# Kernel optimization log

Measured on AMD Instinct MI355X. Metric: run time of the kernel, lower is better.

## Reference

```python
import jax, jax.numpy as jnp
import numpy as np

B, S, V, D, H, T = 16, 256, 32000, 512, 512, 50


def setup_inputs() -> dict:
    key = jax.random.key(0)
    ks = jax.random.split(key, 6)
    tokens = jax.random.randint(ks[0], (B, S), 0, V, dtype=jnp.int64)
    topic_probs = jax.random.uniform(ks[1], (B, S, T), dtype=jnp.float32)
    topic_probs = topic_probs / jnp.linalg.norm(topic_probs, axis=-1, keepdims=True)
    embed_table = jax.random.normal(ks[2], (V, D), dtype=jnp.float32) * 0.02
    lstm_kernel = jax.random.normal(ks[3], (T + D + H, 4 * H), dtype=jnp.float32) * 0.02
    lstm_bias = jnp.zeros((4 * H,), dtype=jnp.float32)
    dense_w = jax.random.normal(ks[4], (H, V), dtype=jnp.float32) * 0.02
    dense_b = jnp.zeros((V,), dtype=jnp.float32)
    return {"tokens": tokens, "topic_probs": topic_probs, "embed_table": embed_table,
            "lstm_kernel": lstm_kernel, "lstm_bias": lstm_bias,
            "dense_w": dense_w, "dense_b": dense_b}


def _lstm(xs, kernel, bias):
    # xs: [B, S, T+D]; TF LSTMCell gate order: i, j(cell cand), f, o; forget_bias=0.0
    h_dim = bias.shape[0] // 4
    b = xs.shape[0]

    def step(carry, xt):
        c, h = carry
        z = jnp.concatenate([xt, h], axis=-1) @ kernel + bias  # [B, 4H]
        i, j, f, o = jnp.split(z, 4, axis=-1)
        c = jax.nn.sigmoid(f) * c + jax.nn.sigmoid(i) * jnp.tanh(j)
        h = jax.nn.sigmoid(o) * jnp.tanh(c)
        return (c, h), h

    init = (jnp.zeros((b, h_dim), xs.dtype), jnp.zeros((b, h_dim), xs.dtype))
    _, hs = jax.lax.scan(step, init, jnp.swapaxes(xs, 0, 1))  # [S, B, H]
    return jnp.swapaxes(hs, 0, 1)


def reference(tokens, topic_probs, embed_table, lstm_kernel, lstm_bias, dense_w, dense_b):
    word_emb = embed_table[tokens]                         # [B, S, D]
    xs = jnp.concatenate([topic_probs, word_emb], axis=-1)  # [B, S, T+D]
    hs = _lstm(xs, lstm_kernel, lstm_bias)                 # [B, S, H]
    logits = hs @ dense_w + dense_b                        # [B, S, V]
    return logits
```

## Files before the change

### kernel.cpp

```cpp
#include <hip/hip_runtime.h>
#include <cstdint>
#include <cstddef>

#define B_ 16
#define S_ 256
#define V_ 32000
#define D_ 512
#define H_ 512
#define T_ 50
#define KX (T_ + D_)
#define G4 (4 * H_)
#define M_ (B_ * S_)

#define GBLK 64
#define NWRK 192
#define UPB 8
#define WST 512
#define NJT 32
#define NNT 250

typedef unsigned short u16;
typedef unsigned int u32;
typedef __attribute__((ext_vector_type(8))) short bf16x8;
typedef __attribute__((ext_vector_type(4))) float f32x4;
typedef __attribute__((ext_vector_type(4))) u16 u16x4;
typedef __attribute__((ext_vector_type(8))) u16 u16x8;
typedef __attribute__((ext_vector_type(4))) u32 u32x4;

__device__ __forceinline__ float sigmoidf_(float x) { return 1.f / (1.f + expf(-x)); }

__device__ __forceinline__ u16 f2bf_rne(float x) {
  u32 u = __float_as_uint(x);
  u32 r = (u + 0x7fffu + ((u >> 16) & 1u)) >> 16;
  return (u16)r;
}
__device__ __forceinline__ float bf2f(u16 h) { return __uint_as_float(((u32)h) << 16); }

__device__ __forceinline__ int swz(int row, int k) {
  return row * WST + (k ^ ((row & 7) << 3));
}

#define GLD_LDS16(g, l) __builtin_amdgcn_global_load_lds( \
    (const __attribute__((address_space(1))) void*)(g), \
    (__attribute__((address_space(3))) void*)(l), 16, 0, 0)

#define BM 128
#define BN 128
#define BK 16

__global__ __launch_bounds__(256) void proj_gemm(
    const int* __restrict__ tokens, const float* __restrict__ topic,
    const float* __restrict__ embed, const float* __restrict__ Wx,
    const float* __restrict__ bias, float* __restrict__ out) {
  __shared__ float As[BK][BM];
  __shared__ float Bs[BK][BN];
  const int tid = threadIdx.x;
  const int bm = blockIdx.y * BM;
  const int bn = blockIdx.x * BN;
  const int tx = tid & 15;
  const int ty = tid >> 4;
  float acc[8][8] = {};

  for (int k0 = 0; k0 < KX; k0 += BK) {
    {
      int r = tid >> 1;
      int kk = (tid & 1) * 8;
      int m = bm + r;
      int tok = tokens[m];
      #pragma unroll
      for (int i = 0; i < 8; ++i) {
        int kg = k0 + kk + i;
        float v = 0.f;
        if (kg < T_)       v = topic[(size_t)m * T_ + kg];
        else if (kg < KX)  v = embed[(size_t)tok * D_ + (kg - T_)];
        As[kk + i][r] = v;
      }
    }
    {
      int kk = tid >> 4;
      int nn = (tid & 15) * 8;
      int kg = k0 + kk;
      const float* Bp = Wx + (size_t)kg * G4 + bn + nn;
      #pragma unroll
      for (int i = 0; i < 8; ++i)
        Bs[kk][nn + i] = (kg < KX) ? Bp[i] : 0.f;
    }
    __syncthreads();
    #pragma unroll
    for (int k = 0; k < BK; ++k) {
      float a[8], bv[8];
      #pragma unroll
      for (int i = 0; i < 8; ++i) a[i] = As[k][ty * 8 + i];
      #pragma unroll
      for (int i = 0; i < 8; ++i) bv[i] = Bs[k][tx * 8 + i];
      #pragma unroll
      for (int i = 0; i < 8; ++i)
        #pragma unroll
        for (int j = 0; j < 8; ++j)
          acc[i][j] += a[i] * bv[j];
    }
    __syncthreads();
  }

  #pragma unroll
  for (int i = 0; i < 8; ++i) {
    int m = bm + ty * 8 + i;
    float* Cp = out + (size_t)m * G4 + bn + tx * 8;
    #pragma unroll
    for (int j = 0; j < 8; ++j)
      Cp[j] = acc[i][j] + bias[bn + tx * 8 + j];
  }
}

__global__ __launch_bounds__(256) void split_w_t(
    const float* __restrict__ W, u16* __restrict__ Whi, u16* __restrict__ Wlo) {
  __shared__ float tile[32][33];
  const int n0 = blockIdx.x * 32, k0 = blockIdx.y * 32;
  const int r = threadIdx.x >> 3;
  const int c4 = (threadIdx.x & 7) * 4;
  const float* src = W + (size_t)(k0 + r) * V_ + n0 + c4;
  #pragma unroll
  for (int i = 0; i < 4; ++i) tile[r][c4 + i] = src[i];
  __syncthreads();
  u16x4 hv, lv;
  #pragma unroll
  for (int i = 0; i < 4; ++i) {
    float x = tile[c4 + i][r];
    u16 h = f2bf_rne(x);
    hv[i] = h;
    lv[i] = f2bf_rne(x - bf2f(h));
  }
  size_t o = (size_t)(n0 + r) * 512 + k0 + c4;
  *(u16x4*)(Whi + o) = hv;
  *(u16x4*)(Wlo + o) = lv;
}

__global__ __launch_bounds__(256, 1) void fused_lstm_dense(
    const float* __restrict__ xs_proj, const float* __restrict__ Wh,
    u32* __restrict__ hpk,
    u32* __restrict__ Apk,
    u32* __restrict__ ctr,
    const u16* __restrict__ Bhi, const u16* __restrict__ Blo,
    const float* __restrict__ bias, float* __restrict__ out) {
  __shared__ u16 whi_l[32 * WST];
  __shared__ u16 wlo_l[32 * WST];
  __shared__ u16 hhi_l[16 * WST];
  __shared__ u16 hlo_l[16 * WST];
  __shared__ float zpart[4][16][34];
  __shared__ u16 Ah_l[128 * 32];
  __shared__ u16 Al_l[128 * 32];
  __shared__ u16 Bh_l[128 * 32];
  __shared__ u16 Bl_l[128 * 32];

  const int bid = blockIdx.x;
  const int tid = threadIdx.x;
  const int w = tid >> 6;
  const int lane = tid & 63;

  if (bid < GBLK) {
    const int u0 = bid * UPB;

    for (int idx = tid; idx < 32 * 512; idx += 256) {
      int c = idx & 31, k = idx >> 5;
      int gc = (c >> 3) * 512 + u0 + (c & 7);
      float v = Wh[(size_t)k * G4 + gc];
      u16 hi = f2bf_rne(v);
      int si = swz(c, k);
      whi_l[si] = hi;
      wlo_l[si] = f2bf_rne(v - bf2f(hi));
    }

    float c_reg = 0.f;
    const int rb = tid >> 3;
    const int rj = tid & 7;
    const int kb = (lane >> 4) * 8;
    const int l15 = lane & 15;

    for (int s = 0; s < S_; ++s) {
      float zi = 0.f, zj2 = 0.f, zf = 0.f, zo = 0.f;
      if (tid < 128) {
        const float* zp = xs_proj + ((size_t)rb * S_ + s) * G4 + u0 + rj;
        zi = zp[0]; zj2 = zp[512]; zf = zp[1024]; zo = zp[1536];
      }

      if (s > 0) {
        if (tid == 0) {
          const u32 tgt = 64u * (u32)s;
          while (__hip_atomic_load(ctr, __ATOMIC_RELAXED,
                                   __HIP_MEMORY_SCOPE_AGENT) < tgt)
            __builtin_amdgcn_s_sleep(1);
        }
        __syncthreads();
        asm volatile("" ::: "memory");
      }

      {
        const u32* src = hpk + (size_t)(s & 1) * 8192;
        u32 v[32];
        #pragma unroll
        for (int j = 0; j < 32; ++j)
          v[j] = __hip_atomic_load(src + tid + j * 256, __ATOMIC_RELAXED,
                                   __HIP_MEMORY_SCOPE_AGENT);
        #pragma unroll
        for (int j = 0; j < 32; ++j) {
          int idx = tid + j * 256;
          int b = idx >> 9, u = idx & 511;
          int si = swz(b, u);
          hhi_l[si] = (u16)(v[j] & 0xffffu);
          hlo_l[si] = (u16)(v[j] >> 16);
        }
      }
      __syncthreads();

      {
        f32x4 acc0 = {0.f, 0.f, 0.f, 0.f};
        f32x4 acc1 = {0.f, 0.f, 0.f, 0.f};
        #pragma unroll
        for (int ks = 0; ks < 4; ++ks) {
          const int k = w * 128 + ks * 32 + kb;
          const int ia = swz(l15, k);
          const int ib = swz(16 + l15, k);
          bf16x8 ah  = *(const bf16x8*)&hhi_l[ia];
          bf16x8 al  = *(const bf16x8*)&hlo_l[ia];
          bf16x8 b0h = *(const bf16x8*)&whi_l[ia];
          bf16x8 b0l = *(const bf16x8*)&wlo_l[ia];
          bf16x8 b1h = *(const bf16x8*)&whi_l[ib];
          bf16x8 b1l = *(const bf16x8*)&wlo_l[ib];
          acc0 = __builtin_amdgcn_mfma_f32_16x16x32_bf16(al, b0h, acc0, 0, 0, 0);
          acc0 = __builtin_amdgcn_mfma_f32_16x16x32_bf16(ah, b0l, acc0, 0, 0, 0);
          acc0 = __builtin_amdgcn_mfma_f32_16x16x32_bf16(ah, b0h, acc0, 0, 0, 0);
          acc1 = __builtin_amdgcn_mfma_f32_16x16x32_bf16(al, b1h, acc1, 0, 0, 0);
          acc1 = __builtin_amdgcn_mfma_f32_16x16x32_bf16(ah, b1l, acc1, 0, 0, 0);
          acc1 = __builtin_amdgcn_mfma_f32_16x16x32_bf16(ah, b1h, acc1, 0, 0, 0);
        }
        #pragma unroll
        for (int jj = 0; jj < 4; ++jj) {
          int r = (lane >> 4) * 4 + jj;
          zpart[w][r][l15] = acc0[jj];
          zpart[w][r][16 + l15] = acc1[jj];
        }
      }
      __syncthreads();

      if (tid < 128) {
        #pragma unroll
        for (int ww = 0; ww < 4; ++ww) {
          zi  += zpart[ww][rb][rj];
          zj2 += zpart[ww][rb][8 + rj];
          zf  += zpart[ww][rb][16 + rj];
          zo  += zpart[ww][rb][24 + rj];
        }
        float cc = sigmoidf_(zf) * c_reg + sigmoidf_(zi) * tanhf(zj2);
        c_reg = cc;
        float h = sigmoidf_(zo) * tanhf(cc);
        u16 hh = f2bf_rne(h);
        u16 hl = f2bf_rne(h - bf2f(hh));
        u32 pack = (u32)hh | ((u32)hl << 16);
        const int hoff = rb * 512 + u0 + rj;
        __hip_atomic_store(hpk + (size_t)((s + 1) & 1) * 8192 + hoff, pack,
                           __ATOMIC_RELAXED, __HIP_MEMORY_SCOPE_AGENT);
        const size_t ar = ((size_t)s * 16 + rb) * 512 + u0 + rj;
        __hip_atomic_store(Apk + ar, pack,
                           __ATOMIC_RELAXED, __HIP_MEMORY_SCOPE_AGENT);
      }
      asm volatile("s_waitcnt vmcnt(0)" ::: "memory");
      __syncthreads();

      if (tid == 0)
        __hip_atomic_fetch_add(ctr, 1u, __ATOMIC_RELAXED,
                               __HIP_MEMORY_SCOPE_AGENT);
    }
  } else {
    const int wid = bid - GBLK;
    const int wm = (w >> 1) * 64, wn = (w & 1) * 64;
    const int l15 = lane & 15;
    const int kb = (lane >> 4) * 8;
    const int lrow = lane >> 2;
    const int lkb = (lane & 3) * 8;
    const int r_ = tid >> 1;
    const int kh = (tid & 1) * 16;

    int lastj = -1;
    for (int t = wid; t < NJT * NNT; t += NWRK) {
      const int jt = t / NNT;
      const int n  = t - jt * NNT;
      if (jt != lastj) {
        if (tid == 0) {
          const u32 tgt = 512u * (u32)(jt + 1);
          while (__hip_atomic_load(ctr, __ATOMIC_RELAXED,
                                   __HIP_MEMORY_SCOPE_AGENT) < tgt)
            __builtin_amdgcn_s_sleep(32);
        }
        __syncthreads();
        asm volatile("" ::: "memory");
        lastj = jt;
      }

      const int bmA = jt * 128;
      const int bn = n * 128;
      f32x4 acc[4][4];
      #pragma unroll
      for (int m = 0; m < 4; ++m)
        #pragma unroll
        for (int q = 0; q < 4; ++q) acc[m][q] = (f32x4){0.f, 0.f, 0.f, 0.f};

      const u16* srcBh = Bhi + (size_t)bn * 512;
      const u16* srcBl = Blo + (size_t)bn * 512;

      for (int k0 = 0; k0 < 512; k0 += 32) {
        {
          const u32* ap = Apk + (size_t)(bmA + r_) * 512 + k0 + kh;
          u32x4 a0 = *(const u32x4*)(ap);
          u32x4 a1 = *(const u32x4*)(ap + 4);
          u32x4 a2 = *(const u32x4*)(ap + 8);
          u32x4 a3 = *(const u32x4*)(ap + 12);
          u16x8 h0, h1, l0, l1;
          #pragma unroll
          for (int i = 0; i < 4; ++i) {
            h0[i]   = (u16)(a0[i] & 0xffffu); l0[i]   = (u16)(a0[i] >> 16);
            h0[4+i] = (u16)(a1[i] & 0xffffu); l0[4+i] = (u16)(a1[i] >> 16);
            h1[i]   = (u16)(a2[i] & 0xffffu); l1[i]   = (u16)(a2[i] >> 16);
            h1[4+i] = (u16)(a3[i] & 0xffffu); l1[4+i] = (u16)(a3[i] >> 16);
          }
          *(u16x8*)&Ah_l[r_ * 32 + kh]     = h0;
          *(u16x8*)&Ah_l[r_ * 32 + kh + 8] = h1;
          *(u16x8*)&Al_l[r_ * 32 + kh]     = l0;
          *(u16x8*)&Al_l[r_ * 32 + kh + 8] = l1;
        }
        #pragma unroll
        for (int cc = 0; cc < 2; ++cc) {
          const int c = w * 2 + cc;
          const int row = c * 16 + lrow;
          const size_t goff = (size_t)row * 512 + k0 + lkb;
          GLD_LDS16(srcBh + goff, &Bh_l[c * 16 * 32]);
          GLD_LDS16(srcBl + goff, &Bl_l[c * 16 * 32]);
        }
        __syncthreads();

        bf16x8 ah[4], al[4], bh[4], bl[4];
        #pragma unroll
        for (int m = 0; m < 4; ++m) {
          int r = wm + m * 16 + l15;
          ah[m] = *(const bf16x8*)&Ah_l[r * 32 + kb];
          al[m] = *(const bf16x8*)&Al_l[r * 32 + kb];
        }
        #pragma unroll
        for (int q = 0; q < 4; ++q) {
          int r = wn + q * 16 + l15;
          bh[q] = *(const bf16x8*)&Bh_l[r * 32 + kb];
          bl[q] = *(const bf16x8*)&Bl_l[r * 32 + kb];
        }
        #pragma unroll
        for (int m = 0; m < 4; ++m)
          #pragma unroll
          for (int q = 0; q < 4; ++q) {
            acc[m][q] = __builtin_amdgcn_mfma_f32_16x16x32_bf16(al[m], bh[q], acc[m][q], 0, 0, 0);
            acc[m][q] = __builtin_amdgcn_mfma_f32_16x16x32_bf16(ah[m], bl[q], acc[m][q], 0, 0, 0);
            acc[m][q] = __builtin_amdgcn_mfma_f32_16x16x32_bf16(ah[m], bh[q], acc[m][q], 0, 0, 0);
          }
        __syncthreads();
      }

      const int lc = lane & 15, lr4 = (lane >> 4) * 4;
      #pragma unroll
      for (int q = 0; q < 4; ++q) {
        int col = bn + wn + q * 16 + lc;
        float bv = bias[col];
        #pragma unroll
        for (int m = 0; m < 4; ++m) {
          int mbase = bmA + wm + m * 16;
          int s = mbase >> 4;
          float* Cp = out + ((size_t)lr4 * 256 + s) * V_ + col;
          #pragma unroll
          for (int jj = 0; jj < 4; ++jj)
            Cp[(size_t)jj * 256 * V_] = acc[m][q][jj] + bv;
        }
      }
    }
  }
}

extern "C" void kernel_launch(void* const* d_in, const int* in_sizes, int n_in,
                              void* d_out, int out_size, void* d_ws, size_t ws_size,
                              hipStream_t stream) {
  const int*   tokens = (const int*)  d_in[0];
  const float* topic  = (const float*)d_in[1];
  const float* embed  = (const float*)d_in[2];
  const float* lk     = (const float*)d_in[3];
  const float* lb     = (const float*)d_in[4];
  const float* dw     = (const float*)d_in[5];
  const float* db     = (const float*)d_in[6];
  float* out = (float*)d_out;

  char* ws = (char*)d_ws;
  size_t off = 0;
  float* xs_proj = (float*)(ws + off); off += (size_t)M_ * G4 * 4;
  u32* Apk = (u32*)(ws + off); off += (size_t)M_ * 512 * 4;
  u16* Whi = (u16*)(ws + off); off += (size_t)V_ * 512 * 2;
  u16* Wlo = (u16*)(ws + off); off += (size_t)V_ * 512 * 2;
  u32* hpk = (u32*)(ws + off); off += 2 * 8192 * 4;
  u32* ctr = (u32*)(ws + off); off += 256;

  hipMemsetAsync(hpk, 0, 2 * 8192 * 4, stream);
  hipMemsetAsync(ctr, 0, 256, stream);

  hipLaunchKernelGGL(split_w_t, dim3(V_ / 32, 512 / 32), dim3(256), 0, stream,
                     dw, Whi, Wlo);

  hipLaunchKernelGGL(proj_gemm, dim3(G4 / BN, M_ / BM), dim3(256), 0, stream,
                     tokens, topic, embed, lk, lb, xs_proj);

  const float* Wh = lk + (size_t)KX * G4;
  hipLaunchKernelGGL(fused_lstm_dense, dim3(GBLK + NWRK), dim3(256), 0, stream,
                     xs_proj, Wh, hpk, Apk, ctr, Whi, Wlo, db, out);
}
```

Baseline: 1.317 ms.

## Move input projection GEMM to split-bf16 MFMA and reorder dense tile loop

Replaces the scalar FP32 input-projection GEMM with a split-precision (hi/lo bf16, three-MFMA) matrix-core kernel. Two new prep kernels gather embeddings and split X into bf16 pairs padded to K=576, and transpose and split the input weights the same way. The X buffers share workspace with the packed h buffer used later. The dense worker loop is also restructured to iterate over time tiles in an outer loop, with work items strided over N inside it. This adds extra prep passes and workspace in exchange for cheaper projection arithmetic.

```diff
diff --git a/kernel.cpp b/kernel.cpp
--- a/kernel.cpp
+++ b/kernel.cpp
@@ -9,6 +9,7 @@
 #define H_ 512
 #define T_ 50
 #define KX (T_ + D_)
+#define KXP 576
 #define G4 (4 * H_)
 #define M_ (B_ * S_)
 
@@ -44,71 +45,131 @@
     (const __attribute__((address_space(1))) void*)(g), \
     (__attribute__((address_space(3))) void*)(l), 16, 0, 0)
 
-#define BM 128
-#define BN 128
-#define BK 16
-
-__global__ __launch_bounds__(256) void proj_gemm(
+__global__ __launch_bounds__(256) void gather_split_x(
     const int* __restrict__ tokens, const float* __restrict__ topic,
-    const float* __restrict__ embed, const float* __restrict__ Wx,
-    const float* __restrict__ bias, float* __restrict__ out) {
-  __shared__ float As[BK][BM];
-  __shared__ float Bs[BK][BN];
+    const float* __restrict__ embed, u16* __restrict__ Xhi,
+    u16* __restrict__ Xlo) {
+  const int m = blockIdx.x;
+  const int tok = tokens[m];
+  const int k4 = threadIdx.x * 4;
+  if (k4 >= KXP) return;
+  u16x4 hv, lv;
+  #pragma unroll
+  for (int i = 0; i < 4; ++i) {
+    int k = k4 + i;
+    float v = 0.f;
+    if (k < T_)       v = topic[(size_t)m * T_ + k];
+    else if (k < KX)  v = embed[(size_t)tok * D_ + (k - T_)];
+    u16 h = f2bf_rne(v);
+    hv[i] = h;
+    lv[i] = f2bf_rne(v - bf2f(h));
+  }
+  size_t o = (size_t)m * KXP + k4;
+  *(u16x4*)(Xhi + o) = hv;
+  *(u16x4*)(Xlo + o) = lv;
+}
+
+__global__ __launch_bounds__(256) void wx_split_t(
+    const float* __restrict__ W, u16* __restrict__ Whi, u16* __restrict__ Wlo) {
+  __shared__ float tile[32][33];
+  const int n0 = blockIdx.x * 32, k0 = blockIdx.y * 32;
+  const int r = threadIdx.x >> 3;
+  const int c4 = (threadIdx.x & 7) * 4;
+  const int kg = k0 + r;
+  const float* src = W + (size_t)kg * G4 + n0 + c4;
+  #pragma unroll
+  for (int i = 0; i < 4; ++i) tile[r][c4 + i] = (kg < KX) ? src[i] : 0.f;
+  __syncthreads();
+  u16x4 hv, lv;
+  #pragma unroll
+  for (int i = 0; i < 4; ++i) {
+    float x = tile[c4 + i][r];
+    u16 h = f2bf_rne(x);
+    hv[i] = h;
+    lv[i] = f2bf_rne(x - bf2f(h));
+  }
+  size_t o = (size_t)(n0 + r) * KXP + k0 + c4;
+  *(u16x4*)(Whi + o) = hv;
+  *(u16x4*)(Wlo + o) = lv;
+}
+
+__global__ __launch_bounds__(256) void proj_mfma(
+    const u16* __restrict__ Ahi, const u16* __restrict__ Alo,
+    const u16* __restrict__ Bhi, const u16* __restrict__ Blo,
+    const float* __restrict__ bias, float* __restrict__ C) {
+  __shared__ u16 lds[4][128 * 32];
   const int tid = threadIdx.x;
-  const int bm = blockIdx.y * BM;
-  const int bn = blockIdx.x * BN;
-  const int tx = tid & 15;
-  const int ty = tid >> 4;
-  float acc[8][8] = {};
-
-  for (int k0 = 0; k0 < KX; k0 += BK) {
-    {
-      int r = tid >> 1;
-      int kk = (tid & 1) * 8;
-      int m = bm + r;
-      int tok = tokens[m];
+  const int w = tid >> 6, lane = tid & 63;
+  const int bm = blockIdx.y * 128;
+  const int bn = blockIdx.x * 128;
+  const int wm = (w >> 1) * 64, wn = (w & 1) * 64;
+
+  f32x4 acc[4][4];
+  #pragma unroll
+  for (int m = 0; m < 4; ++m)
+    #pragma unroll
+    for (int n = 0; n < 4; ++n) acc[m][n] = (f32x4){0.f, 0.f, 0.f, 0.f};
+
+  const u16* src0 = Ahi + (size_t)bm * KXP;
+  const u16* src1 = Alo + (size_t)bm * KXP;
+  const u16* src2 = Bhi + (size_t)bn * KXP;
+  const u16* src3 = Blo + (size_t)bn * KXP;
+
+  const int lrow = lane >> 2;
+  const int lkb  = (lane & 3) * 8;
+  const int kb   = (lane >> 4) * 8;
+
+  for (int k0 = 0; k0 < KXP; k0 += 32) {
+    #pragma unroll
+    for (int cc = 0; cc < 2; ++cc) {
+      const int c = w * 2 + cc;
+      const int row = c * 16 + lrow;
+      const size_t goff = (size_t)row * KXP + k0 + lkb;
+      u16* l = &lds[0][0] + c * 16 * 32;
+      GLD_LDS16(src0 + goff, l);
+      GLD_LDS16(src1 + goff, l + 128 * 32);
+      GLD_LDS16(src2 + goff, l + 2 * 128 * 32);
+      GLD_LDS16(src3 + goff, l + 3 * 128 * 32);
+    }
+    __syncthreads();
+
+    bf16x8 ah[4], al[4], bh[4], bl[4];
+    #pragma unroll
+    for (int m = 0; m < 4; ++m) {
+      int r = wm + m * 16 + (lane & 15);
+      ah[m] = *(const bf16x8*)&lds[0][r * 32 + kb];
+      al[m] = *(const bf16x8*)&lds[1][r * 32 + kb];
+    }
+    #pragma unroll
+    for (int n = 0; n < 4; ++n) {
+      int r = wn + n * 16 + (lane & 15);
+      bh[n] = *(const bf16x8*)&lds[2][r * 32 + kb];
+      bl[n] = *(const bf16x8*)&lds[3][r * 32 + kb];
+    }
+    #pragma unroll
+    for (int m = 0; m < 4; ++m)
       #pragma unroll
-      for (int i = 0; i < 8; ++i) {
-        int kg = k0 + kk + i;
-        float v = 0.f;
-        if (kg < T_)       v = topic[(size_t)m * T_ + kg];
-        else if (kg < KX)  v = embed[(size_t)tok * D_ + (kg - T_)];
-        As[kk + i][r] = v;
-      }
-    }
-    {
-      int kk = tid >> 4;
-      int nn = (tid & 15) * 8;
-      int kg = k0 + kk;
-      const float* Bp = Wx + (size_t)kg * G4 + bn + nn;
+      for (int n = 0; n < 4; ++n) {
+        acc[m][n] = __builtin_amdgcn_mfma_f32_16x16x32_bf16(al[m], bh[n], acc[m][n], 0, 0, 0);
+        acc[m][n] = __builtin_amdgcn_mfma_f32_16x16x32_bf16(ah[m], bl[n], acc[m][n], 0, 0, 0);
+        acc[m][n] = __builtin_amdgcn_mfma_f32_16x16x32_bf16(ah[m], bh[n], acc[m][n], 0, 0, 0);
+      }
+    __syncthreads();
+  }
+
+  const int lc = lane & 15, lr4 = (lane >> 4) * 4;
+  #pragma unroll
+  for (int n = 0; n < 4; ++n) {
+    int col = bn + wn + n * 16 + lc;
+    float bv = bias[col];
+    #pragma unroll
+    for (int m = 0; m < 4; ++m) {
+      int row0 = bm + wm + m * 16 + lr4;
+      float* Cp = C + (size_t)row0 * G4 + col;
       #pragma unroll
-      for (int i = 0; i < 8; ++i)
-        Bs[kk][nn + i] = (kg < KX) ? Bp[i] : 0.f;
-    }
-    __syncthreads();
-    #pragma unroll
-    for (int k = 0; k < BK; ++k) {
-      float a[8], bv[8];
-      #pragma unroll
-      for (int i = 0; i < 8; ++i) a[i] = As[k][ty * 8 + i];
-      #pragma unroll
-      for (int i = 0; i < 8; ++i) bv[i] = Bs[k][tx * 8 + i];
-      #pragma unroll
-      for (int i = 0; i < 8; ++i)
-        #pragma unroll
-        for (int j = 0; j < 8; ++j)
-          acc[i][j] += a[i] * bv[j];
-    }
-    __syncthreads();
-  }
-
-  #pragma unroll
-  for (int i = 0; i < 8; ++i) {
-    int m = bm + ty * 8 + i;
-    float* Cp = out + (size_t)m * G4 + bn + tx * 8;
-    #pragma unroll
-    for (int j = 0; j < 8; ++j)
-      Cp[j] = acc[i][j] + bias[bn + tx * 8 + j];
+      for (int j = 0; j < 4; ++j)
+        Cp[(size_t)j * G4] = acc[m][n][j] + bv;
+    }
   }
 }
 
@@ -280,100 +341,96 @@
     const int r_ = tid >> 1;
     const int kh = (tid & 1) * 16;
 
-    int lastj = -1;
-    for (int t = wid; t < NJT * NNT; t += NWRK) {
-      const int jt = t / NNT;
-      const int n  = t - jt * NNT;
-      if (jt != lastj) {
-        if (tid == 0) {
-          const u32 tgt = 512u * (u32)(jt + 1);
-          while (__hip_atomic_load(ctr, __ATOMIC_RELAXED,
-                                   __HIP_MEMORY_SCOPE_AGENT) < tgt)
-            __builtin_amdgcn_s_sleep(32);
-        }
-        __syncthreads();
-        asm volatile("" ::: "memory");
-        lastj = jt;
-      }
+    for (int jt = 0; jt < NJT; ++jt) {
+      if (tid == 0) {
+        const u32 tgt = 512u * (u32)(jt + 1);
+        while (__hip_atomic_load(ctr, __ATOMIC_RELAXED,
+                                 __HIP_MEMORY_SCOPE_AGENT) < tgt)
+          __builtin_amdgcn_s_sleep(32);
+      }
+      __syncthreads();
+      asm volatile("" ::: "memory");
 
       const int bmA = jt * 128;
-      const int bn = n * 128;
-      f32x4 acc[4][4];
-      #pragma unroll
-      for (int m = 0; m < 4; ++m)
-        #pragma unroll
-        for (int q = 0; q < 4; ++q) acc[m][q] = (f32x4){0.f, 0.f, 0.f, 0.f};
-
-      const u16* srcBh = Bhi + (size_t)bn * 512;
-      const u16* srcBl = Blo + (size_t)bn * 512;
-
-      for (int k0 = 0; k0 < 512; k0 += 32) {
-        {
-          const u32* ap = Apk + (size_t)(bmA + r_) * 512 + k0 + kh;
-          u32x4 a0 = *(const u32x4*)(ap);
-          u32x4 a1 = *(const u32x4*)(ap + 4);
-          u32x4 a2 = *(const u32x4*)(ap + 8);
-          u32x4 a3 = *(const u32x4*)(ap + 12);
-          u16x8 h0, h1, l0, l1;
-          #pragma unroll
-          for (int i = 0; i < 4; ++i) {
-            h0[i]   = (u16)(a0[i] & 0xffffu); l0[i]   = (u16)(a0[i] >> 16);
-            h0[4+i] = (u16)(a1[i] & 0xffffu); l0[4+i] = (u16)(a1[i] >> 16);
-            h1[i]   = (u16)(a2[i] & 0xffffu); l1[i]   = (u16)(a2[i] >> 16);
-            h1[4+i] = (u16)(a3[i] & 0xffffu); l1[4+i] = (u16)(a3[i] >> 16);
+      for (int n = wid; n < NNT; n += NWRK) {
+        const int bn = n * 128;
+        f32x4 acc[4][4];
+        #pragma unroll
+        for (int m = 0; m < 4; ++m)
+          #pragma unroll
+          for (int q = 0; q < 4; ++q) acc[m][q] = (f32x4){0.f, 0.f, 0.f, 0.f};
+
+        const u16* srcBh = Bhi + (size_t)bn * 512;
+        const u16* srcBl = Blo + (size_t)bn * 512;
+
+        for (int k0 = 0; k0 < 512; k0 += 32) {
+          {
+            const u32* ap = Apk + (size_t)(bmA + r_) * 512 + k0 + kh;
+            u32x4 a0 = *(const u32x4*)(ap);
+            u32x4 a1 = *(const u32x4*)(ap + 4);
+            u32x4 a2 = *(const u32x4*)(ap + 8);
+            u32x4 a3 = *(const u32x4*)(ap + 12);
+            u16x8 h0, h1, l0, l1;
+            #pragma unroll
+            for (int i = 0; i < 4; ++i) {
+              h0[i]   = (u16)(a0[i] & 0xffffu); l0[i]   = (u16)(a0[i] >> 16);
+              h0[4+i] = (u16)(a1[i] & 0xffffu); l0[4+i] = (u16)(a1[i] >> 16);
+              h1[i]   = (u16)(a2[i] & 0xffffu); l1[i]   = (u16)(a2[i] >> 16);
+              h1[4+i] = (u16)(a3[i] & 0xffffu); l1[4+i] = (u16)(a3[i] >> 16);
+            }
+            *(u16x8*)&Ah_l[r_ * 32 + kh]     = h0;
+            *(u16x8*)&Ah_l[r_ * 32 + kh + 8] = h1;
+            *(u16x8*)&Al_l[r_ * 32 + kh]     = l0;
+            *(u16x8*)&Al_l[r_ * 32 + kh + 8] = l1;
           }
-          *(u16x8*)&Ah_l[r_ * 32 + kh]     = h0;
-          *(u16x8*)&Ah_l[r_ * 32 + kh + 8] = h1;
-          *(u16x8*)&Al_l[r_ * 32 + kh]     = l0;
-          *(u16x8*)&Al_l[r_ * 32 + kh + 8] = l1;
-        }
-        #pragma unroll
-        for (int cc = 0; cc < 2; ++cc) {
-          const int c = w * 2 + cc;
-          const int row = c * 16 + lrow;
-          const size_t goff = (size_t)row * 512 + k0 + lkb;
-          GLD_LDS16(srcBh + goff, &Bh_l[c * 16 * 32]);
-          GLD_LDS16(srcBl + goff, &Bl_l[c * 16 * 32]);
-        }
-        __syncthreads();
-
-        bf16x8 ah[4], al[4], bh[4], bl[4];
-        #pragma unroll
-        for (int m = 0; m < 4; ++m) {
-          int r = wm + m * 16 + l15;
-          ah[m] = *(const bf16x8*)&Ah_l[r * 32 + kb];
-          al[m] = *(const bf16x8*)&Al_l[r * 32 + kb];
-        }
+          #pragma unroll
+          for (int cc = 0; cc < 2; ++cc) {
+            const int c = w * 2 + cc;
+            const int row = c * 16 + lrow;
+            const size_t goff = (size_t)row * 512 + k0 + lkb;
+            GLD_LDS16(srcBh + goff, &Bh_l[c * 16 * 32]);
+            GLD_LDS16(srcBl + goff, &Bl_l[c * 16 * 32]);
+          }
+          __syncthreads();
+
+          bf16x8 ah[4], al[4], bh[4], bl[4];
+          #pragma unroll
+          for (int m = 0; m < 4; ++m) {
+            int r = wm + m * 16 + l15;
+            ah[m] = *(const bf16x8*)&Ah_l[r * 32 + kb];
+            al[m] = *(const bf16x8*)&Al_l[r * 32 + kb];
+          }
+          #pragma unroll
+          for (int q = 0; q < 4; ++q) {
+            int r = wn + q * 16 + l15;
+            bh[q] = *(const bf16x8*)&Bh_l[r * 32 + kb];
+            bl[q] = *(const bf16x8*)&Bl_l[r * 32 + kb];
+          }
+          #pragma unroll
+          for (int m = 0; m < 4; ++m)
+            #pragma unroll
+            for (int q = 0; q < 4; ++q) {
+              acc[m][q] = __builtin_amdgcn_mfma_f32_16x16x32_bf16(al[m], bh[q], acc[m][q], 0, 0, 0);
+              acc[m][q] = __builtin_amdgcn_mfma_f32_16x16x32_bf16(ah[m], bl[q], acc[m][q], 0, 0, 0);
+              acc[m][q] = __builtin_amdgcn_mfma_f32_16x16x32_bf16(ah[m], bh[q], acc[m][q], 0, 0, 0);
+            }
+          __syncthreads();
+        }
+
+        const int lc = lane & 15, lr4 = (lane >> 4) * 4;
         #pragma unroll
         for (int q = 0; q < 4; ++q) {
-          int r = wn + q * 16 + l15;
-          bh[q] = *(const bf16x8*)&Bh_l[r * 32 + kb];
-          bl[q] = *(const bf16x8*)&Bl_l[r * 32 + kb];
-        }
-        #pragma unroll
-        for (int m = 0; m < 4; ++m)
-          #pragma unroll
-          for (int q = 0; q < 4; ++q) {
-            acc[m][q] = __builtin_amdgcn_mfma_f32_16x16x32_bf16(al[m], bh[q], acc[m][q], 0, 0, 0);
-            acc[m][q] = __builtin_amdgcn_mfma_f32_16x16x32_bf16(ah[m], bl[q], acc[m][q], 0, 0, 0);
-            acc[m][q] = __builtin_amdgcn_mfma_f32_16x16x32_bf16(ah[m], bh[q], acc[m][q], 0, 0, 0);
+          int col = bn + wn + q * 16 + lc;
+          float bv = bias[col];
+          #pragma unroll
+          for (int m = 0; m < 4; ++m) {
+            int mbase = bmA + wm + m * 16;
+            int s = mbase >> 4;
+            float* Cp = out + ((size_t)lr4 * 256 + s) * V_ + col;
+            #pragma unroll
+            for (int jj = 0; jj < 4; ++jj)
+              Cp[(size_t)jj * 256 * V_] = acc[m][q][jj] + bv;
           }
-        __syncthreads();
-      }
-
-      const int lc = lane & 15, lr4 = (lane >> 4) * 4;
-      #pragma unroll
-      for (int q = 0; q < 4; ++q) {
-        int col = bn + wn + q * 16 + lc;
-        float bv = bias[col];
-        #pragma unroll
-        for (int m = 0; m < 4; ++m) {
-          int mbase = bmA + wm + m * 16;
-          int s = mbase >> 4;
-          float* Cp = out + ((size_t)lr4 * 256 + s) * V_ + col;
-          #pragma unroll
-          for (int jj = 0; jj < 4; ++jj)
-            Cp[(size_t)jj * 256 * V_] = acc[m][q][jj] + bv;
         }
       }
     }
@@ -395,9 +452,15 @@
   char* ws = (char*)d_ws;
   size_t off = 0;
   float* xs_proj = (float*)(ws + off); off += (size_t)M_ * G4 * 4;
-  u32* Apk = (u32*)(ws + off); off += (size_t)M_ * 512 * 4;
+  char* xa = ws + off;
+  u16* Xhi = (u16*)xa;
+  u16* Xlo = (u16*)(xa + (size_t)M_ * KXP * 2);
+  u32* Apk = (u32*)xa;
+  off += (size_t)M_ * KXP * 2 * 2;
   u16* Whi = (u16*)(ws + off); off += (size_t)V_ * 512 * 2;
   u16* Wlo = (u16*)(ws + off); off += (size_t)V_ * 512 * 2;
+  u16* Wxhi = (u16*)(ws + off); off += (size_t)G4 * KXP * 2;
+  u16* Wxlo = (u16*)(ws + off); off += (size_t)G4 * KXP * 2;
   u32* hpk = (u32*)(ws + off); off += 2 * 8192 * 4;
   u32* ctr = (u32*)(ws + off); off += 256;
 
@@ -406,9 +469,13 @@
 
   hipLaunchKernelGGL(split_w_t, dim3(V_ / 32, 512 / 32), dim3(256), 0, stream,
                      dw, Whi, Wlo);
-
-  hipLaunchKernelGGL(proj_gemm, dim3(G4 / BN, M_ / BM), dim3(256), 0, stream,
-                     tokens, topic, embed, lk, lb, xs_proj);
+  hipLaunchKernelGGL(wx_split_t, dim3(G4 / 32, KXP / 32), dim3(256), 0, stream,
+                     lk, Wxhi, Wxlo);
+  hipLaunchKernelGGL(gather_split_x, dim3(M_), dim3(256), 0, stream,
+                     tokens, topic, embed, Xhi, Xlo);
+
+  hipLaunchKernelGGL(proj_mfma, dim3(G4 / 128, M_ / 128), dim3(256), 0, stream,
+                     Xhi, Xlo, Wxhi, Wxlo, lb, xs_proj);
 
   const float* Wh = lk + (size_t)KX * G4;
   hipLaunchKernelGGL(fused_lstm_dense, dim3(GBLK + NWRK), dim3(256), 0, stream,
```

After: 1.685 ms. +27.9%, slower.
